# Performance work log

Hardware: AMD Instinct MI355X
Metric: run time of the kernel (lower is better)

The kernel has to match this reference:

```python
import jax, jax.numpy as jnp
import numpy as np
import math

IN_FEATURES = 4096
OUT_FEATURES = 4096
P = max(IN_FEATURES, OUT_FEATURES)   # total_permutations
D = min(IN_FEATURES, OUT_FEATURES)   # diag_length
SPARSITY = 0.1
K = math.ceil(int((1.0 - SPARSITY) * IN_FEATURES * OUT_FEATURES) / D)  # 3687
ALPHA_LR = 0.01
NUM_ITER = 50


def sparse_soft_topk_mask_dykstra(alpha, k, l, num_iter):
    """Dykstra projection of alpha/l onto {0<=m<=1, sum(m)=k} (soft top-k mask)."""
    s = alpha / l
    n = s.shape[0]
    p0 = jnp.zeros_like(s)
    q0 = jnp.zeros_like(s)

    def body(carry, _):
        x, p, q = carry
        # project x+p onto hyperplane sum = k
        t = x + p
        y = t + (k - jnp.sum(t)) / n
        p = t - y
        # project y+q onto box [0, 1]
        u = y + q
        x_new = jnp.clip(u, 0.0, 1.0)
        q = u - x_new
        return (x_new, p, q), None

    (x, _, _), _ = jax.lax.scan(body, (s, p0, q0), None, length=num_iter)
    return x  # last projection is onto the box -> exact zeros / ones


def compute_weight(V, alpha):
    a = sparse_soft_topk_mask_dykstra(alpha, K, ALPHA_LR, NUM_ITER)  # (P,)
    vals = a[:, None] * V                                             # (P, D)
    i = jnp.arange(P)[:, None]
    j = jnp.arange(D)[None, :]
    if OUT_FEATURES >= IN_FEATURES:
        # pseudo-diagonal i: rows shifted by i, column j scaled by V[i, j]
        rows = (i + j) % OUT_FEATURES
        cols = jnp.broadcast_to(j, (P, D))
    else:
        # row r scaled by V[i, r], columns shifted by i
        rows = jnp.broadcast_to(j, (P, D))
        cols = (i + j) % IN_FEATURES
    W = jnp.zeros((OUT_FEATURES, IN_FEATURES), V.dtype)
    W = W.at[rows.reshape(-1), cols.reshape(-1)].add(vals.reshape(-1))
    return W


def setup_inputs() -> dict:
    key = jax.random.key(0)
    k1, k2 = jax.random.split(key)
    # kaiming_uniform_(a=sqrt(5)) over fan_in = D -> bound = sqrt(1/D)
    bound = 1.0 / np.sqrt(D)
    V = jax.random.uniform(k1, (P, D), jnp.float32, -bound, bound)
    alpha = jnp.ones((P,), jnp.float32) / IN_FEATURES
    x = jax.random.normal(k2, (512, IN_FEATURES), jnp.float32)
    return {"x": x, "V": V, "alpha": alpha}


def reference(x, V, alpha):
    W = compute_weight(V, alpha)  # (out, in)
    return x @ W.T                # F.linear(x, W)
```

## Files before the change

### kernel.cpp

```cpp
#include <hip/hip_runtime.h>
#include <hip/hip_bf16.h>
#include <stdint.h>

#define PDIM 4096
#define KSEL 3687.0f
#define NITER 50

typedef unsigned short ushort_t;
typedef __attribute__((ext_vector_type(8))) __bf16 bf16x8;
typedef __attribute__((ext_vector_type(4))) float f32x4;

typedef __attribute__((address_space(3))) void lds_void;
typedef __attribute__((address_space(1))) const void glob_void;

__device__ __forceinline__ ushort_t f32_to_bf16_rne(float f) {
  union { float f; uint32_t u; } v; v.f = f;
  uint32_t r = 0x7FFFu + ((v.u >> 16) & 1u);
  return (ushort_t)((v.u + r) >> 16);
}

__device__ __forceinline__ void async_cp16(const void* g, void* l) {
  __builtin_amdgcn_global_load_lds((glob_void*)g, (lds_void*)l, 16, 0, 0);
}

__global__ __launch_bounds__(256) void prep_kernel(
    const float* __restrict__ alpha, float* __restrict__ a_out,
    const float* __restrict__ x, ushort_t* __restrict__ Xb, int n4) {
  if (blockIdx.x != 0) {
    const int i = (blockIdx.x - 1) * 256 + threadIdx.x;
    if (i < n4) {
      const float4 v = ((const float4*)x)[i];
      ushort4 o;
      o.x = f32_to_bf16_rne(v.x);
      o.y = f32_to_bf16_rne(v.y);
      o.z = f32_to_bf16_rne(v.z);
      o.w = f32_to_bf16_rne(v.w);
      ((ushort4*)Xb)[i] = o;
    }
    return;
  }
  __shared__ float red[8];
  const int tid = threadIdx.x;
  const int lane = tid & 63;
  const int wv = tid >> 6;
  float xx[16], q[16];
  float p = 0.0f;
#pragma unroll
  for (int i = 0; i < 16; ++i) {
    xx[i] = alpha[i * 256 + tid] * 100.0f;
    q[i] = 0.0f;
  }
  for (int it = 0; it < NITER; ++it) {
    float t[16];
    float loc = 0.0f;
#pragma unroll
    for (int i = 0; i < 16; ++i) { t[i] = xx[i] + p; loc += t[i]; }
#pragma unroll
    for (int off = 32; off > 0; off >>= 1) loc += __shfl_down(loc, off, 64);
    const int slot = (it & 1) * 4;
    if (lane == 0) red[slot + wv] = loc;
    __syncthreads();
    const float tot = red[slot] + red[slot + 1] + red[slot + 2] + red[slot + 3];
    const float corr = (KSEL - tot) * (1.0f / 4096.0f);
    p = -corr;
#pragma unroll
    for (int i = 0; i < 16; ++i) {
      const float y = t[i] + corr;
      const float u = y + q[i];
      const float xn = fminf(fmaxf(u, 0.0f), 1.0f);
      q[i] = u - xn;
      xx[i] = xn;
    }
  }
#pragma unroll
  for (int i = 0; i < 16; ++i) a_out[i * 256 + tid] = xx[i];
}

__global__ __launch_bounds__(256) void wmat_kernel(
    const float* __restrict__ V, const float* __restrict__ a,
    ushort_t* __restrict__ Wb) {
  __shared__ float vt[192][67];
  const int t = threadIdx.x;
  const int r0 = blockIdx.x * 128;
  const int c0 = blockIdx.y * 64;
  const int dbase = (r0 - c0 - 63 + 2 * PDIM) & (PDIM - 1);
  const int csub = (t & 15) * 4;
  const int rsub = t >> 4;
#pragma unroll
  for (int i = 0; i < 12; ++i) {
    const int ld = i * 16 + rsub;
    const int d = (dbase + ld) & (PDIM - 1);
    const float av = a[d];
    const float4 vv = *(const float4*)(V + (size_t)d * PDIM + c0 + csub);
    vt[ld][csub + 0] = av * vv.x;
    vt[ld][csub + 1] = av * vv.y;
    vt[ld][csub + 2] = av * vv.z;
    vt[ld][csub + 3] = av * vv.w;
  }
  __syncthreads();
#pragma unroll
  for (int k = 0; k < 4; ++k) {
    const int ry = (t >> 3) + k * 32;
    const int cb = (t & 7) * 8;
    ushort_t pk[8];
#pragma unroll
    for (int j = 0; j < 8; ++j) {
      const int c = cb + j;
      pk[j] = f32_to_bf16_rne(vt[ry - c + 63][c]);
    }
    *(uint4*)(Wb + (size_t)(r0 + ry) * PDIM + c0 + cb) = *(const uint4*)pk;
  }
}

__global__ __launch_bounds__(256) void gemm_kernel(
    const ushort_t* __restrict__ Xb, const ushort_t* __restrict__ Wb,
    float* __restrict__ par, int M) {
  constexpr int Kdim = 4096, Ndim = 4096, KQ = 1024;
  __shared__ __align__(16) ushort_t As[64 * 64];
  __shared__ __align__(16) ushort_t Bs[128 * 64];
  const int tid = threadIdx.x;
  const int lane = tid & 63;
  const int w = tid >> 6;
  const int l15 = lane & 15;
  const int quad = lane >> 4;
  const int m0 = blockIdx.y * 64;
  const int n0 = blockIdx.x * 128;
  const int kbase = blockIdx.z * KQ;
  float* outp = par + (size_t)blockIdx.z * ((size_t)512 * Ndim);
  const int arow = lane >> 3;
  const int aslot = lane & 7;

  f32x4 acc[4][2];
#pragma unroll
  for (int mt = 0; mt < 4; ++mt)
#pragma unroll
    for (int nt = 0; nt < 2; ++nt) acc[mt][nt] = (f32x4){0.f, 0.f, 0.f, 0.f};

  for (int it = 0; it < KQ / 64; ++it) {
    const int k0 = kbase + it * 64;
#pragma unroll
    for (int s = w; s < 8; s += 4) {
      const int row = s * 8 + arow;
      const int j = aslot ^ (row & 7);
      async_cp16(Xb + (size_t)(m0 + row) * Kdim + k0 + j * 8,
                 (char*)As + (size_t)s * 1024);
    }
#pragma unroll
    for (int s = w; s < 16; s += 4) {
      const int row = s * 8 + arow;
      const int j = aslot ^ (row & 7);
      async_cp16(Wb + (size_t)(n0 + row) * Kdim + k0 + j * 8,
                 (char*)Bs + (size_t)s * 1024);
    }
    __syncthreads();
#pragma unroll
    for (int kk = 0; kk < 64; kk += 32) {
      const int cj = (kk >> 3) + quad;
      bf16x8 af[4], bfv[2];
#pragma unroll
      for (int mt = 0; mt < 4; ++mt) {
        const int row = mt * 16 + l15;
        af[mt] = *(const bf16x8*)&As[(row * 8 + (cj ^ (row & 7))) * 8];
      }
#pragma unroll
      for (int nt = 0; nt < 2; ++nt) {
        const int row = w * 32 + nt * 16 + l15;
        bfv[nt] = *(const bf16x8*)&Bs[(row * 8 + (cj ^ (row & 7))) * 8];
      }
#pragma unroll
      for (int mt = 0; mt < 4; ++mt)
#pragma unroll
        for (int nt = 0; nt < 2; ++nt)
          acc[mt][nt] = __builtin_amdgcn_mfma_f32_16x16x32_bf16(
              af[mt], bfv[nt], acc[mt][nt], 0, 0, 0);
    }
    __syncthreads();
  }
#pragma unroll
  for (int mt = 0; mt < 4; ++mt) {
#pragma unroll
    for (int nt = 0; nt < 2; ++nt) {
      const int mb = m0 + mt * 16 + quad * 4;
      const int n = n0 + w * 32 + nt * 16 + l15;
#pragma unroll
      for (int r = 0; r < 4; ++r)
        outp[(size_t)(mb + r) * Ndim + n] = acc[mt][nt][r];
    }
  }
}

__global__ __launch_bounds__(256) void combine_kernel(
    const float4* __restrict__ par, float4* __restrict__ out, int n4) {
  const int i = blockIdx.x * 256 + threadIdx.x;
  if (i >= n4) return;
  const float4 a = par[i];
  const float4 b = par[i + n4];
  const float4 c = par[i + 2 * n4];
  const float4 d = par[i + 3 * n4];
  float4 o;
  o.x = (a.x + b.x) + (c.x + d.x);
  o.y = (a.y + b.y) + (c.y + d.y);
  o.z = (a.z + b.z) + (c.z + d.z);
  o.w = (a.w + b.w) + (c.w + d.w);
  out[i] = o;
}

extern "C" void kernel_launch(void* const* d_in, const int* in_sizes, int n_in,
                              void* d_out, int out_size, void* d_ws,
                              size_t ws_size, hipStream_t stream) {
  const float* x = (const float*)d_in[0];
  const float* V = (const float*)d_in[1];
  const float* alpha = (const float*)d_in[2];
  float* out = (float*)d_out;
  const int M = in_sizes[0] / PDIM;

  float* a_mask = (float*)d_ws;
  ushort_t* Xb = (ushort_t*)((char*)d_ws + 16 * 1024);
  ushort_t* Wb = Xb + (size_t)M * PDIM;
  float* par = (float*)(Wb + (size_t)PDIM * PDIM);

  const int n4x = (M * PDIM) / 4;
  prep_kernel<<<1 + (n4x + 255) / 256, 256, 0, stream>>>(alpha, a_mask, x, Xb,
                                                         n4x);
  wmat_kernel<<<dim3(PDIM / 128, PDIM / 64), 256, 0, stream>>>(V, a_mask, Wb);
  gemm_kernel<<<dim3(PDIM / 128, M / 64, 4), 256, 0, stream>>>(Xb, Wb, par, M);
  const int n4o = out_size / 4;
  combine_kernel<<<(n4o + 255) / 256, 256, 0, stream>>>((const float4*)par,
                                                        (float4*)out, n4o);
}
```

Before: 164.8 us.

## Enlarge GEMM tile to 128x128 with 8-way split-K and retile weight build

The GEMM block tile grows from 64x128 to 128x128, the split-K factor goes from 4 to 8, and occupancy is hinted at 3 blocks per CU; the combine kernel now sums 8 partial buffers. The goal is better operand reuse per block, so each loaded tile feeds more MFMAs and L2/LDS traffic per flop drops. The weight-construction kernel is retiled to 256x32 output tiles, which cuts redundant diagonal rows of V loaded per tile. In exchange, the fp32 partial-sum traffic written and read by combine doubles, and the workspace must hold 8 partial buffers.

```diff
diff --git a/kernel.cpp b/kernel.cpp
--- a/kernel.cpp
+++ b/kernel.cpp
@@ -79,76 +79,73 @@
 __global__ __launch_bounds__(256) void wmat_kernel(
     const float* __restrict__ V, const float* __restrict__ a,
     ushort_t* __restrict__ Wb) {
-  __shared__ float vt[192][67];
+  __shared__ float vt[287][34];
   const int t = threadIdx.x;
-  const int r0 = blockIdx.x * 128;
-  const int c0 = blockIdx.y * 64;
-  const int dbase = (r0 - c0 - 63 + 2 * PDIM) & (PDIM - 1);
-  const int csub = (t & 15) * 4;
-  const int rsub = t >> 4;
-#pragma unroll
-  for (int i = 0; i < 12; ++i) {
-    const int ld = i * 16 + rsub;
-    const int d = (dbase + ld) & (PDIM - 1);
-    const float av = a[d];
-    const float4 vv = *(const float4*)(V + (size_t)d * PDIM + c0 + csub);
-    vt[ld][csub + 0] = av * vv.x;
-    vt[ld][csub + 1] = av * vv.y;
-    vt[ld][csub + 2] = av * vv.z;
-    vt[ld][csub + 3] = av * vv.w;
+  const int r0 = blockIdx.x * 256;
+  const int c0 = blockIdx.y * 32;
+  const int dbase = (r0 - c0 - 31 + 2 * PDIM) & (PDIM - 1);
+  const int cs = (t & 7) * 4;
+  const int rsub = t >> 3;
+#pragma unroll
+  for (int i = 0; i < 9; ++i) {
+    const int ld = i * 32 + rsub;
+    if (ld < 287) {
+      const int d = (dbase + ld) & (PDIM - 1);
+      const float av = a[d];
+      const float4 vv = *(const float4*)(V + (size_t)d * PDIM + c0 + cs);
+      vt[ld][cs + 0] = av * vv.x;
+      vt[ld][cs + 1] = av * vv.y;
+      vt[ld][cs + 2] = av * vv.z;
+      vt[ld][cs + 3] = av * vv.w;
+    }
   }
   __syncthreads();
+  const int cb = (t & 3) * 8;
 #pragma unroll
   for (int k = 0; k < 4; ++k) {
-    const int ry = (t >> 3) + k * 32;
-    const int cb = (t & 7) * 8;
+    const int ry = k * 64 + (t >> 2);
     ushort_t pk[8];
 #pragma unroll
     for (int j = 0; j < 8; ++j) {
       const int c = cb + j;
-      pk[j] = f32_to_bf16_rne(vt[ry - c + 63][c]);
+      pk[j] = f32_to_bf16_rne(vt[ry - c + 31][c]);
     }
     *(uint4*)(Wb + (size_t)(r0 + ry) * PDIM + c0 + cb) = *(const uint4*)pk;
   }
 }
 
-__global__ __launch_bounds__(256) void gemm_kernel(
+__global__ __launch_bounds__(256, 3) void gemm_kernel(
     const ushort_t* __restrict__ Xb, const ushort_t* __restrict__ Wb,
     float* __restrict__ par, int M) {
-  constexpr int Kdim = 4096, Ndim = 4096, KQ = 1024;
-  __shared__ __align__(16) ushort_t As[64 * 64];
+  constexpr int Kdim = 4096, Ndim = 4096, KQ = 512;
+  __shared__ __align__(16) ushort_t As[128 * 64];
   __shared__ __align__(16) ushort_t Bs[128 * 64];
   const int tid = threadIdx.x;
   const int lane = tid & 63;
   const int w = tid >> 6;
   const int l15 = lane & 15;
   const int quad = lane >> 4;
-  const int m0 = blockIdx.y * 64;
+  const int m0 = blockIdx.y * 128;
   const int n0 = blockIdx.x * 128;
   const int kbase = blockIdx.z * KQ;
   float* outp = par + (size_t)blockIdx.z * ((size_t)512 * Ndim);
   const int arow = lane >> 3;
   const int aslot = lane & 7;
 
-  f32x4 acc[4][2];
-#pragma unroll
-  for (int mt = 0; mt < 4; ++mt)
+  f32x4 acc[8][2];
+#pragma unroll
+  for (int mt = 0; mt < 8; ++mt)
 #pragma unroll
     for (int nt = 0; nt < 2; ++nt) acc[mt][nt] = (f32x4){0.f, 0.f, 0.f, 0.f};
 
   for (int it = 0; it < KQ / 64; ++it) {
     const int k0 = kbase + it * 64;
 #pragma unroll
-    for (int s = w; s < 8; s += 4) {
+    for (int s = w; s < 16; s += 4) {
       const int row = s * 8 + arow;
       const int j = aslot ^ (row & 7);
       async_cp16(Xb + (size_t)(m0 + row) * Kdim + k0 + j * 8,
                  (char*)As + (size_t)s * 1024);
-    }
-#pragma unroll
-    for (int s = w; s < 16; s += 4) {
-      const int row = s * 8 + arow;
-      const int j = aslot ^ (row & 7);
       async_cp16(Wb + (size_t)(n0 + row) * Kdim + k0 + j * 8,
                  (char*)Bs + (size_t)s * 1024);
     }
@@ -156,28 +153,26 @@
 #pragma unroll
     for (int kk = 0; kk < 64; kk += 32) {
       const int cj = (kk >> 3) + quad;
-      bf16x8 af[4], bfv[2];
-#pragma unroll
-      for (int mt = 0; mt < 4; ++mt) {
-        const int row = mt * 16 + l15;
-        af[mt] = *(const bf16x8*)&As[(row * 8 + (cj ^ (row & 7))) * 8];
-      }
+      bf16x8 bfv[2];
 #pragma unroll
       for (int nt = 0; nt < 2; ++nt) {
         const int row = w * 32 + nt * 16 + l15;
         bfv[nt] = *(const bf16x8*)&Bs[(row * 8 + (cj ^ (row & 7))) * 8];
       }
 #pragma unroll
-      for (int mt = 0; mt < 4; ++mt)
-#pragma unroll
-        for (int nt = 0; nt < 2; ++nt)
-          acc[mt][nt] = __builtin_amdgcn_mfma_f32_16x16x32_bf16(
-              af[mt], bfv[nt], acc[mt][nt], 0, 0, 0);
+      for (int mt = 0; mt < 8; ++mt) {
+        const int row = mt * 16 + l15;
+        const bf16x8 af = *(const bf16x8*)&As[(row * 8 + (cj ^ (row & 7))) * 8];
+        acc[mt][0] = __builtin_amdgcn_mfma_f32_16x16x32_bf16(af, bfv[0],
+                                                             acc[mt][0], 0, 0, 0);
+        acc[mt][1] = __builtin_amdgcn_mfma_f32_16x16x32_bf16(af, bfv[1],
+                                                             acc[mt][1], 0, 0, 0);
+      }
     }
     __syncthreads();
   }
 #pragma unroll
-  for (int mt = 0; mt < 4; ++mt) {
+  for (int mt = 0; mt < 8; ++mt) {
 #pragma unroll
     for (int nt = 0; nt < 2; ++nt) {
       const int mb = m0 + mt * 16 + quad * 4;
@@ -193,15 +188,23 @@
     const float4* __restrict__ par, float4* __restrict__ out, int n4) {
   const int i = blockIdx.x * 256 + threadIdx.x;
   if (i >= n4) return;
-  const float4 a = par[i];
-  const float4 b = par[i + n4];
-  const float4 c = par[i + 2 * n4];
-  const float4 d = par[i + 3 * n4];
+  float4 s0 = par[i];
+  float4 s1 = par[i + n4];
+  float4 s2 = par[i + 2 * n4];
+  float4 s3 = par[i + 3 * n4];
+#pragma unroll
+  for (int z = 4; z < 8; ++z) {
+    const float4 v = par[i + (size_t)z * n4];
+    if (z == 4) { s0.x += v.x; s0.y += v.y; s0.z += v.z; s0.w += v.w; }
+    if (z == 5) { s1.x += v.x; s1.y += v.y; s1.z += v.z; s1.w += v.w; }
+    if (z == 6) { s2.x += v.x; s2.y += v.y; s2.z += v.z; s2.w += v.w; }
+    if (z == 7) { s3.x += v.x; s3.y += v.y; s3.z += v.z; s3.w += v.w; }
+  }
   float4 o;
-  o.x = (a.x + b.x) + (c.x + d.x);
-  o.y = (a.y + b.y) + (c.y + d.y);
-  o.z = (a.z + b.z) + (c.z + d.z);
-  o.w = (a.w + b.w) + (c.w + d.w);
+  o.x = (s0.x + s1.x) + (s2.x + s3.x);
+  o.y = (s0.y + s1.y) + (s2.y + s3.y);
+  o.z = (s0.z + s1.z) + (s2.z + s3.z);
+  o.w = (s0.w + s1.w) + (s2.w + s3.w);
   out[i] = o;
 }
 
@@ -222,8 +225,8 @@
   const int n4x = (M * PDIM) / 4;
   prep_kernel<<<1 + (n4x + 255) / 256, 256, 0, stream>>>(alpha, a_mask, x, Xb,
                                                          n4x);
-  wmat_kernel<<<dim3(PDIM / 128, PDIM / 64), 256, 0, stream>>>(V, a_mask, Wb);
-  gemm_kernel<<<dim3(PDIM / 128, M / 64, 4), 256, 0, stream>>>(Xb, Wb, par, M);
+  wmat_kernel<<<dim3(PDIM / 256, PDIM / 32), 256, 0, stream>>>(V, a_mask, Wb);
+  gemm_kernel<<<dim3(PDIM / 128, M / 128, 8), 256, 0, stream>>>(Xb, Wb, par, M);
   const int n4o = out_size / 4;
   combine_kernel<<<(n4o + 255) / 256, 256, 0, stream>>>((const float4*)par,
                                                         (float4*)out, n4o);
```

After: 178.2 us. 1.08x slower.

## Split-K into 8 slices with bf16 tile-contiguous partials and fragment-order combine

Applied to the files above, without the earlier changes.

The GEMM now splits K into 8 slices of 512 instead of 4 of 1024, doubling the grid for more parallelism. Each block stores its partial sums as bf16 in its register-fragment order, so writes are contiguous. The combine kernel reads the 8 bf16 partials per tile and writes the fp32 output. This cuts partial-sum traffic and improves coalescing and occupancy, but rounding partials to bf16 adds error to the final sum. The grid order also changes so the K slices sit in x.

```diff
diff --git a/kernel.cpp b/kernel.cpp
--- a/kernel.cpp
+++ b/kernel.cpp
@@ -17,6 +17,11 @@
   union { float f; uint32_t u; } v; v.f = f;
   uint32_t r = 0x7FFFu + ((v.u >> 16) & 1u);
   return (ushort_t)((v.u + r) >> 16);
+}
+
+__device__ __forceinline__ float bf16_to_f32(ushort_t h) {
+  union { uint32_t u; float f; } v; v.u = ((uint32_t)h) << 16;
+  return v.f;
 }
 
 __device__ __forceinline__ void async_cp16(const void* g, void* l) {
@@ -114,8 +119,8 @@
 
 __global__ __launch_bounds__(256) void gemm_kernel(
     const ushort_t* __restrict__ Xb, const ushort_t* __restrict__ Wb,
-    float* __restrict__ par, int M) {
-  constexpr int Kdim = 4096, Ndim = 4096, KQ = 1024;
+    ushort_t* __restrict__ par) {
+  constexpr int Kdim = 4096, KQ = 512;
   __shared__ __align__(16) ushort_t As[64 * 64];
   __shared__ __align__(16) ushort_t Bs[128 * 64];
   const int tid = threadIdx.x;
@@ -123,10 +128,12 @@
   const int w = tid >> 6;
   const int l15 = lane & 15;
   const int quad = lane >> 4;
-  const int m0 = blockIdx.y * 64;
-  const int n0 = blockIdx.x * 128;
-  const int kbase = blockIdx.z * KQ;
-  float* outp = par + (size_t)blockIdx.z * ((size_t)512 * Ndim);
+  const int z = blockIdx.x;
+  const int nblk = blockIdx.y;
+  const int mblk = blockIdx.z;
+  const int m0 = mblk * 64;
+  const int n0 = nblk * 128;
+  const int kbase = z * KQ;
   const int arow = lane >> 3;
   const int aslot = lane & 7;
 
@@ -176,33 +183,56 @@
     }
     __syncthreads();
   }
+  const int tile = nblk * 8 + mblk;
+  ushort_t* pbase = par + ((size_t)z * 256 + tile) * 8192;
 #pragma unroll
   for (int mt = 0; mt < 4; ++mt) {
 #pragma unroll
     for (int nt = 0; nt < 2; ++nt) {
-      const int mb = m0 + mt * 16 + quad * 4;
-      const int n = n0 + w * 32 + nt * 16 + l15;
-#pragma unroll
-      for (int r = 0; r < 4; ++r)
-        outp[(size_t)(mb + r) * Ndim + n] = acc[mt][nt][r];
+      const int slot = mt * 2 + nt;
+      ushort4 o;
+      o.x = f32_to_bf16_rne(acc[mt][nt][0]);
+      o.y = f32_to_bf16_rne(acc[mt][nt][1]);
+      o.z = f32_to_bf16_rne(acc[mt][nt][2]);
+      o.w = f32_to_bf16_rne(acc[mt][nt][3]);
+      *(ushort4*)(pbase + (size_t)(slot * 256 + tid) * 4) = o;
     }
   }
 }
 
 __global__ __launch_bounds__(256) void combine_kernel(
-    const float4* __restrict__ par, float4* __restrict__ out, int n4) {
-  const int i = blockIdx.x * 256 + threadIdx.x;
-  if (i >= n4) return;
-  const float4 a = par[i];
-  const float4 b = par[i + n4];
-  const float4 c = par[i + 2 * n4];
-  const float4 d = par[i + 3 * n4];
-  float4 o;
-  o.x = (a.x + b.x) + (c.x + d.x);
-  o.y = (a.y + b.y) + (c.y + d.y);
-  o.z = (a.z + b.z) + (c.z + d.z);
-  o.w = (a.w + b.w) + (c.w + d.w);
-  out[i] = o;
+    const ushort_t* __restrict__ par, float* __restrict__ out) {
+  const int tile = blockIdx.x;
+  const int nblk = tile >> 3;
+  const int mblk = tile & 7;
+  const int m0 = mblk * 64;
+  const int n0 = nblk * 128;
+  const int tid = threadIdx.x;
+  const int lane = tid & 63;
+  const int w = tid >> 6;
+  const int l15 = lane & 15;
+  const int quad = lane >> 4;
+#pragma unroll
+  for (int slot = 0; slot < 8; ++slot) {
+    float s0 = 0.f, s1 = 0.f, s2 = 0.f, s3 = 0.f;
+#pragma unroll
+    for (int z = 0; z < 8; ++z) {
+      const ushort4 v = *(const ushort4*)(par +
+          ((size_t)z * 256 + tile) * 8192 + (size_t)(slot * 256 + tid) * 4);
+      s0 += bf16_to_f32(v.x);
+      s1 += bf16_to_f32(v.y);
+      s2 += bf16_to_f32(v.z);
+      s3 += bf16_to_f32(v.w);
+    }
+    const int mt = slot >> 1;
+    const int nt = slot & 1;
+    const int mb = m0 + mt * 16 + quad * 4;
+    const int n = n0 + w * 32 + nt * 16 + l15;
+    out[(size_t)(mb + 0) * PDIM + n] = s0;
+    out[(size_t)(mb + 1) * PDIM + n] = s1;
+    out[(size_t)(mb + 2) * PDIM + n] = s2;
+    out[(size_t)(mb + 3) * PDIM + n] = s3;
+  }
 }
 
 extern "C" void kernel_launch(void* const* d_in, const int* in_sizes, int n_in,
@@ -217,14 +247,12 @@
   float* a_mask = (float*)d_ws;
   ushort_t* Xb = (ushort_t*)((char*)d_ws + 16 * 1024);
   ushort_t* Wb = Xb + (size_t)M * PDIM;
-  float* par = (float*)(Wb + (size_t)PDIM * PDIM);
+  ushort_t* par = Wb + (size_t)PDIM * PDIM;
 
   const int n4x = (M * PDIM) / 4;
   prep_kernel<<<1 + (n4x + 255) / 256, 256, 0, stream>>>(alpha, a_mask, x, Xb,
                                                          n4x);
   wmat_kernel<<<dim3(PDIM / 128, PDIM / 64), 256, 0, stream>>>(V, a_mask, Wb);
-  gemm_kernel<<<dim3(PDIM / 128, M / 64, 4), 256, 0, stream>>>(Xb, Wb, par, M);
-  const int n4o = out_size / 4;
-  combine_kernel<<<(n4o + 255) / 256, 256, 0, stream>>>((const float4*)par,
-                                                        (float4*)out, n4o);
-}
+  gemm_kernel<<<dim3(8, PDIM / 128, M / 64), 256, 0, stream>>>(Xb, Wb, par);
+  combine_kernel<<<256, 256, 0, stream>>>(par, out);
+}
```

Result: no change. 164.2 us (-0.3%).
